# Kernel optimization log

Hardware: AMD Instinct MI355X
Metric: run time of the kernel (lower is better)

## Reference

```python
import jax, jax.numpy as jnp
import numpy as np

DIM = 384
HEADS = 6
K = 3  # kernel_size, stride = 1


def setup_inputs() -> dict:
    key = jax.random.key(0)
    ks = jax.random.split(key, 7)
    B, H, W, C = 16, 56, 56, DIM
    sc = 1.0 / np.sqrt(C)
    return {
        "x_map": jax.random.normal(ks[0], (B, H, W, C), dtype=jnp.float32),
        # Linear weights stored [in, out] (torch stores [out, in]; math identical)
        "W_attn": jax.random.normal(ks[1], (C, HEADS * K * K), dtype=jnp.float32) * sc,
        "b_attn": jax.random.normal(ks[2], (HEADS * K * K,), dtype=jnp.float32) * 0.02,
        "W_v": jax.random.normal(ks[3], (C, C), dtype=jnp.float32) * sc,
        "b_v": jax.random.normal(ks[4], (C,), dtype=jnp.float32) * 0.02,
        "W_proj": jax.random.normal(ks[5], (C, C), dtype=jnp.float32) * sc,
        "b_proj": jax.random.normal(ks[6], (C,), dtype=jnp.float32) * 0.02,
    }


def reference(x_map, W_attn, b_attn, W_v, b_v, W_proj, b_proj):
    B, H, W, C = x_map.shape
    k, heads = K, HEADS
    hd = C // heads
    pad = k // 2

    # attention logits per output pixel: [B, H*W, heads, k*k], softmax over window
    a = x_map @ W_attn + b_attn                     # [B,H,W,heads*k*k]
    a = jax.nn.softmax(a.reshape(B, H * W, heads, k * k), axis=-1)

    v = x_map @ W_v + b_v                           # [B,H,W,C]
    vp = jnp.pad(v, ((0, 0), (pad, pad), (pad, pad), (0, 0)))
    # k*k shifted views == F.unfold with row-major (ki,kj) kernel order
    patches = jnp.stack(
        [vp[:, i:i + H, j:j + W, :] for i in range(k) for j in range(k)],
        axis=3,
    )                                               # [B,H,W,k*k,C]
    patches = patches.reshape(B, H * W, k * k, heads, hd)

    # softmax-weighted sum over the k*k window, per head
    y = jnp.einsum('bpKhd,bphK->bphd', patches, a)  # [B,H*W,heads,hd]
    y = y.reshape(B, H, W, C)
    return y @ W_proj + b_proj
```

## Files before the change

kernel.cpp:

```cpp
#include <hip/hip_runtime.h>
#include <math.h>

#define NPIX 50176
#define CDIM 384
#define HEADS 6
#define NLOGIT 54
#define HH 56
#define WW 56

typedef __attribute__((ext_vector_type(8))) __bf16 bf16x8;
typedef __attribute__((ext_vector_type(4))) float f32x4;

__device__ __forceinline__ void glds16(const void* g, void* l) {
  __builtin_amdgcn_global_load_lds(
      (const __attribute__((address_space(1))) unsigned int*)g,
      (__attribute__((address_space(3))) unsigned int*)l, 16, 0, 0);
}

__global__ __launch_bounds__(256) void prep_kernel(
    const float* __restrict__ W_v, const float* __restrict__ W_proj,
    const float* __restrict__ W_attn, const float* __restrict__ b_attn,
    __bf16* __restrict__ Wtv, __bf16* __restrict__ Wtp,
    __bf16* __restrict__ Wta, float* __restrict__ bpad) {
  const int idx = blockIdx.x * 256 + threadIdx.x;
  const int WSZ = CDIM * CDIM;
  if (idx < WSZ) {
    const int n = idx / CDIM, k = idx % CDIM;
    Wtv[idx] = (__bf16)W_v[k * CDIM + n];
    Wtp[idx] = (__bf16)W_proj[k * CDIM + n];
  } else if (idx < WSZ + 64 * CDIM) {
    const int r = idx - WSZ;
    const int n = r / CDIM, k = r % CDIM;
    Wta[r] = (__bf16)((n < NLOGIT) ? W_attn[k * NLOGIT + n] : 0.f);
  } else if (idx < WSZ + 64 * CDIM + 64) {
    const int n = idx - WSZ - 64 * CDIM;
    bpad[n] = (n < NLOGIT) ? b_attn[n] : 0.f;
  }
}

__global__ __launch_bounds__(256) void cast_x_kernel(
    const float* __restrict__ x, __bf16* __restrict__ xb) {
  const size_t i = (size_t)blockIdx.x * 256 + threadIdx.x;
  const float4* src = (const float4*)x + i * 4;
  const float4 f0 = src[0];
  const float4 f1 = src[1];
  const float4 f2 = src[2];
  const float4 f3 = src[3];
  bf16x8 o0, o1;
  o0[0] = (__bf16)f0.x; o0[1] = (__bf16)f0.y; o0[2] = (__bf16)f0.z; o0[3] = (__bf16)f0.w;
  o0[4] = (__bf16)f1.x; o0[5] = (__bf16)f1.y; o0[6] = (__bf16)f1.z; o0[7] = (__bf16)f1.w;
  o1[0] = (__bf16)f2.x; o1[1] = (__bf16)f2.y; o1[2] = (__bf16)f2.z; o1[3] = (__bf16)f2.w;
  o1[4] = (__bf16)f3.x; o1[5] = (__bf16)f3.y; o1[6] = (__bf16)f3.z; o1[7] = (__bf16)f3.w;
  ((bf16x8*)xb)[i * 2]     = o0;
  ((bf16x8*)xb)[i * 2 + 1] = o1;
}

__global__ __launch_bounds__(256) void gemm_v_logit_kernel(
    const __bf16* __restrict__ xb, const __bf16* __restrict__ Wtv,
    const float* __restrict__ b_v, __bf16* __restrict__ v,
    const __bf16* __restrict__ Wta, const float* __restrict__ bpad,
    float* __restrict__ attn) {
  __shared__ char smem[34816];
  __bf16 (*As)[32] = (__bf16(*)[32])smem;
  __bf16 (*Bs)[32] = (__bf16(*)[32])(smem + 8192);
  float (*Ls)[68]  = (float(*)[68])smem;

  const int tid  = threadIdx.x;
  const int wave = tid >> 6;
  const int lane = tid & 63;
  const int bm   = blockIdx.x * 128;
  const int lrow  = lane >> 2;
  const int lkoff = (lane & 3) * 8;
  const int frow  = lane & 15;
  const int fk    = (lane >> 4) * 8;

  if (blockIdx.y < 3) {
    const int bn = blockIdx.y * 128;
    const int wr = (wave >> 1) * 64;
    const int wc = (wave & 1) * 64;
    f32x4 acc[4][4] = {};

    for (int k0 = 0; k0 < CDIM; k0 += 32) {
      const __bf16* ga = xb  + (size_t)(bm + wave * 32 + lrow) * CDIM + k0 + lkoff;
      const __bf16* gb = Wtv + (size_t)(bn + wave * 32 + lrow) * CDIM + k0 + lkoff;
      glds16(ga,                     &As[wave * 32][0]);
      glds16(ga + 16 * (size_t)CDIM, &As[wave * 32 + 16][0]);
      glds16(gb,                     &Bs[wave * 32][0]);
      glds16(gb + 16 * (size_t)CDIM, &Bs[wave * 32 + 16][0]);
      __syncthreads();

      bf16x8 a[4], b[4];
      #pragma unroll
      for (int mi = 0; mi < 4; ++mi)
        a[mi] = *(const bf16x8*)&As[wr + mi * 16 + frow][fk];
      #pragma unroll
      for (int ni = 0; ni < 4; ++ni)
        b[ni] = *(const bf16x8*)&Bs[wc + ni * 16 + frow][fk];
      #pragma unroll
      for (int mi = 0; mi < 4; ++mi)
        #pragma unroll
        for (int ni = 0; ni < 4; ++ni)
          acc[mi][ni] = __builtin_amdgcn_mfma_f32_16x16x32_bf16(
              a[mi], b[ni], acc[mi][ni], 0, 0, 0);
      __syncthreads();
    }

    const int orow = (lane >> 4) * 4;
    #pragma unroll
    for (int mi = 0; mi < 4; ++mi) {
      #pragma unroll
      for (int ni = 0; ni < 4; ++ni) {
        const int n = bn + wc + ni * 16 + frow;
        const float bvl = b_v[n];
        #pragma unroll
        for (int r = 0; r < 4; ++r) {
          const int m = bm + wr + mi * 16 + orow + r;
          v[(size_t)m * CDIM + n] = (__bf16)(acc[mi][ni][r] + bvl);
        }
      }
    }
  } else {
    f32x4 acc[2][4] = {};

    for (int k0 = 0; k0 < CDIM; k0 += 32) {
      const __bf16* ga = xb  + (size_t)(bm + wave * 32 + lrow) * CDIM + k0 + lkoff;
      const __bf16* gb = Wta + (size_t)(wave * 16 + lrow) * CDIM + k0 + lkoff;
      glds16(ga,                     &As[wave * 32][0]);
      glds16(ga + 16 * (size_t)CDIM, &As[wave * 32 + 16][0]);
      glds16(gb,                     &Bs[wave * 16][0]);
      __syncthreads();

      bf16x8 a[2], b[4];
      #pragma unroll
      for (int mi = 0; mi < 2; ++mi)
        a[mi] = *(const bf16x8*)&As[wave * 32 + mi * 16 + frow][fk];
      #pragma unroll
      for (int ni = 0; ni < 4; ++ni)
        b[ni] = *(const bf16x8*)&Bs[ni * 16 + frow][fk];
      #pragma unroll
      for (int mi = 0; mi < 2; ++mi)
        #pragma unroll
        for (int ni = 0; ni < 4; ++ni)
          acc[mi][ni] = __builtin_amdgcn_mfma_f32_16x16x32_bf16(
              a[mi], b[ni], acc[mi][ni], 0, 0, 0);
      __syncthreads();
    }

    float bvl[4];
    #pragma unroll
    for (int ni = 0; ni < 4; ++ni) bvl[ni] = bpad[ni * 16 + frow];
    const int orow = (lane >> 4) * 4;
    #pragma unroll
    for (int mi = 0; mi < 2; ++mi)
      #pragma unroll
      for (int ni = 0; ni < 4; ++ni)
        #pragma unroll
        for (int r = 0; r < 4; ++r)
          Ls[wave * 32 + mi * 16 + orow + r][ni * 16 + frow] =
              acc[mi][ni][r] + bvl[ni];
    __syncthreads();

    #pragma unroll
    for (int it = 0; it < 3; ++it) {
      const int task = it * 256 + tid;
      const int pl = task / HEADS;
      const int h  = task % HEADS;
      const float* row = &Ls[pl][h * 9];
      float m = row[0];
      #pragma unroll
      for (int w = 1; w < 9; ++w) m = fmaxf(m, row[w]);
      float e[9], s = 0.f;
      #pragma unroll
      for (int w = 0; w < 9; ++w) { e[w] = __expf(row[w] - m); s += e[w]; }
      const float inv = 1.f / s;
      float* op = &attn[(size_t)(bm + pl) * NLOGIT + h * 9];
      #pragma unroll
      for (int w = 0; w < 9; ++w) op[w] = e[w] * inv;
    }
  }
}

__global__ __launch_bounds__(256) void gemm_proj_kernel(
    const __bf16* __restrict__ A, const __bf16* __restrict__ Bt,
    const float* __restrict__ bias, float* __restrict__ Out) {
  __shared__ __bf16 As[128][32];
  __shared__ __bf16 Bs[128][32];

  const int tid  = threadIdx.x;
  const int wave = tid >> 6;
  const int lane = tid & 63;
  const int bm = blockIdx.x * 128;
  const int bn = blockIdx.y * 128;

  const int lrow  = lane >> 2;
  const int lkoff = (lane & 3) * 8;
  const int frow  = lane & 15;
  const int fk    = (lane >> 4) * 8;
  const int wr = (wave >> 1) * 64;
  const int wc = (wave & 1) * 64;

  f32x4 acc[4][4] = {};

  for (int k0 = 0; k0 < CDIM; k0 += 32) {
    const __bf16* ga = A  + (size_t)(bm + wave * 32 + lrow) * CDIM + k0 + lkoff;
    const __bf16* gb = Bt + (size_t)(bn + wave * 32 + lrow) * CDIM + k0 + lkoff;
    glds16(ga,                     &As[wave * 32][0]);
    glds16(ga + 16 * (size_t)CDIM, &As[wave * 32 + 16][0]);
    glds16(gb,                     &Bs[wave * 32][0]);
    glds16(gb + 16 * (size_t)CDIM, &Bs[wave * 32 + 16][0]);
    __syncthreads();

    bf16x8 a[4], b[4];
    #pragma unroll
    for (int mi = 0; mi < 4; ++mi)
      a[mi] = *(const bf16x8*)&As[wr + mi * 16 + frow][fk];
    #pragma unroll
    for (int ni = 0; ni < 4; ++ni)
      b[ni] = *(const bf16x8*)&Bs[wc + ni * 16 + frow][fk];
    #pragma unroll
    for (int mi = 0; mi < 4; ++mi)
      #pragma unroll
      for (int ni = 0; ni < 4; ++ni)
        acc[mi][ni] = __builtin_amdgcn_mfma_f32_16x16x32_bf16(
            a[mi], b[ni], acc[mi][ni], 0, 0, 0);
    __syncthreads();
  }

  const int orow = (lane >> 4) * 4;
  #pragma unroll
  for (int mi = 0; mi < 4; ++mi) {
    #pragma unroll
    for (int ni = 0; ni < 4; ++ni) {
      const int n = bn + wc + ni * 16 + frow;
      const float bvl = bias[n];
      #pragma unroll
      for (int r = 0; r < 4; ++r) {
        const int m = bm + wr + mi * 16 + orow + r;
        Out[(size_t)m * CDIM + n] = acc[mi][ni][r] + bvl;
      }
    }
  }
}

__global__ __launch_bounds__(256) void aggregate_kernel(
    const __bf16* __restrict__ v, const float* __restrict__ attn,
    __bf16* __restrict__ y) {
  const int idx = blockIdx.x * 256 + threadIdx.x;
  const int cg = idx % 48;
  const int pg = idx / 48;
  const int c  = cg * 8;
  const int b  = pg / ((HH / 4) * WW);
  const int r2 = pg % ((HH / 4) * WW);
  const int i0 = (r2 / WW) * 4;
  const int j  = r2 % WW;
  const int head = c >> 6;

  const int pbase = (b * HH + i0) * WW + j;
  float aw[4][9];
  #pragma unroll
  for (int p = 0; p < 4; ++p) {
    const float* ap = attn + (size_t)(pbase + p * WW) * NLOGIT + head * 9;
    #pragma unroll
    for (int w = 0; w < 9; ++w) aw[p][w] = ap[w];
  }

  const bool j0ok = (j > 0), j2ok = (j < WW - 1);
  float acc[4][8] = {};

  #pragma unroll
  for (int li = 0; li < 6; ++li) {
    const int ii = i0 - 1 + li;
    if (ii < 0 || ii >= HH) continue;
    const __bf16* vrow = v + ((size_t)(b * HH + ii) * WW + j) * CDIM + c;
    float ch[3][8];
    #pragma unroll
    for (int kj = 0; kj < 3; ++kj) {
      const bool ok = (kj == 0) ? j0ok : (kj == 2) ? j2ok : true;
      if (ok) {
        const bf16x8 vv = *(const bf16x8*)(vrow + (kj - 1) * CDIM);
        #pragma unroll
        for (int q = 0; q < 8; ++q) ch[kj][q] = (float)vv[q];
      } else {
        #pragma unroll
        for (int q = 0; q < 8; ++q) ch[kj][q] = 0.f;
      }
    }
    #pragma unroll
    for (int p = 0; p < 4; ++p) {
      const int ki = li - p;
      if (ki < 0 || ki > 2) continue;
      #pragma unroll
      for (int kj = 0; kj < 3; ++kj) {
        const float w = aw[p][ki * 3 + kj];
        #pragma unroll
        for (int q = 0; q < 8; ++q) acc[p][q] += w * ch[kj][q];
      }
    }
  }

  #pragma unroll
  for (int p = 0; p < 4; ++p) {
    bf16x8 o;
    #pragma unroll
    for (int q = 0; q < 8; ++q) o[q] = (__bf16)acc[p][q];
    *(bf16x8*)&y[(size_t)(pbase + p * WW) * CDIM + c] = o;
  }
}

extern "C" void kernel_launch(void* const* d_in, const int* in_sizes, int n_in,
                              void* d_out, int out_size, void* d_ws,
                              size_t ws_size, hipStream_t stream) {
  const float* x      = (const float*)d_in[0];
  const float* W_attn = (const float*)d_in[1];
  const float* b_attn = (const float*)d_in[2];
  const float* W_v    = (const float*)d_in[3];
  const float* b_v    = (const float*)d_in[4];
  const float* W_proj = (const float*)d_in[5];
  const float* b_proj = (const float*)d_in[6];
  float* out = (float*)d_out;

  char* w = (char*)d_ws;
  __bf16* xb   = (__bf16*)w;  w += (size_t)NPIX * CDIM * 2;
  __bf16* v    = (__bf16*)w;  w += (size_t)NPIX * CDIM * 2;
  __bf16* y    = (__bf16*)w;  w += (size_t)NPIX * CDIM * 2;
  float*  attn = (float*)w;   w += (size_t)NPIX * NLOGIT * 4;
  __bf16* Wta  = (__bf16*)w;  w += 64 * CDIM * 2;
  float*  bpad = (float*)w;   w += 64 * 4;
  __bf16* Wtv  = (__bf16*)w;  w += CDIM * CDIM * 2;
  __bf16* Wtp  = (__bf16*)w;  w += CDIM * CDIM * 2;

  const int prep_n = CDIM * CDIM + 64 * CDIM + 64;
  prep_kernel<<<(prep_n + 255) / 256, 256, 0, stream>>>(
      W_v, W_proj, W_attn, b_attn, Wtv, Wtp, Wta, bpad);

  cast_x_kernel<<<(NPIX * CDIM / 16) / 256, 256, 0, stream>>>(x, xb);

  gemm_v_logit_kernel<<<dim3(NPIX / 128, 4), 256, 0, stream>>>(
      xb, Wtv, b_v, v, Wta, bpad, attn);

  aggregate_kernel<<<(NPIX / 4 * 48) / 256, 256, 0, stream>>>(v, attn, y);

  gemm_proj_kernel<<<dim3(NPIX / 128, CDIM / 128), 256, 0, stream>>>(
      y, Wtp, b_proj, out);
}
```

Measured before the change: 119.7 us.

## Fuse window aggregation into projection GEMM A-tile construction

Removes the separate aggregate kernel and the intermediate y buffer by computing each softmax-weighted 3x3 window sum directly into the shared-memory A tile of the projection GEMM. This saves a full write and read of the bf16 y tensor and one kernel launch. In exchange, the aggregation is recomputed once per output-column block (three times) and the neighbor gathers sit on the GEMM critical path without row reuse.

```diff
diff --git a/kernel.cpp b/kernel.cpp
--- a/kernel.cpp
+++ b/kernel.cpp
@@ -180,9 +180,10 @@
   }
 }
 
-__global__ __launch_bounds__(256) void gemm_proj_kernel(
-    const __bf16* __restrict__ A, const __bf16* __restrict__ Bt,
-    const float* __restrict__ bias, float* __restrict__ Out) {
+__global__ __launch_bounds__(256) void gemm_proj_agg_kernel(
+    const __bf16* __restrict__ v, const float* __restrict__ attn,
+    const __bf16* __restrict__ Bt, const float* __restrict__ bias,
+    float* __restrict__ Out) {
   __shared__ __bf16 As[128][32];
   __shared__ __bf16 Bs[128][32];
 
@@ -199,15 +200,64 @@
   const int wr = (wave >> 1) * 64;
   const int wc = (wave & 1) * 64;
 
+  const int px0 = tid >> 2;
+  const int cg  = tid & 3;
+  int ibase[2], jpos[2];
+  size_t vbase[2];
+  #pragma unroll
+  for (int t = 0; t < 2; ++t) {
+    const int p = bm + px0 + t * 64;
+    const int bimg = p / (HH * WW);
+    const int rem  = p % (HH * WW);
+    ibase[t] = rem / WW;
+    jpos[t]  = rem % WW;
+    vbase[t] = ((size_t)(bimg * HH + ibase[t]) * WW + jpos[t]) * CDIM;
+  }
+
+  float aw[2][9];
   f32x4 acc[4][4] = {};
 
-  for (int k0 = 0; k0 < CDIM; k0 += 32) {
-    const __bf16* ga = A  + (size_t)(bm + wave * 32 + lrow) * CDIM + k0 + lkoff;
+  for (int ks = 0; ks < 12; ++ks) {
+    const int k0 = ks * 32;
     const __bf16* gb = Bt + (size_t)(bn + wave * 32 + lrow) * CDIM + k0 + lkoff;
-    glds16(ga,                     &As[wave * 32][0]);
-    glds16(ga + 16 * (size_t)CDIM, &As[wave * 32 + 16][0]);
     glds16(gb,                     &Bs[wave * 32][0]);
     glds16(gb + 16 * (size_t)CDIM, &Bs[wave * 32 + 16][0]);
+
+    if ((ks & 1) == 0) {
+      const int head = k0 >> 6;
+      #pragma unroll
+      for (int t = 0; t < 2; ++t) {
+        const int p = bm + px0 + t * 64;
+        const float* ap = attn + (size_t)p * NLOGIT + head * 9;
+        #pragma unroll
+        for (int w = 0; w < 9; ++w) aw[t][w] = ap[w];
+      }
+    }
+
+    #pragma unroll
+    for (int t = 0; t < 2; ++t) {
+      const int i = ibase[t], j = jpos[t];
+      float a8[8] = {};
+      #pragma unroll
+      for (int ki = 0; ki < 3; ++ki) {
+        const int ii = i + ki - 1;
+        if (ii < 0 || ii >= HH) continue;
+        #pragma unroll
+        for (int kj = 0; kj < 3; ++kj) {
+          const int jj = j + kj - 1;
+          if (jj < 0 || jj >= WW) continue;
+          const float wgt = aw[t][ki * 3 + kj];
+          const bf16x8 vv = *(const bf16x8*)&v[
+              vbase[t] + ((ii - i) * WW + (jj - j)) * CDIM + k0 + cg * 8];
+          #pragma unroll
+          for (int q = 0; q < 8; ++q) a8[q] += wgt * (float)vv[q];
+        }
+      }
+      bf16x8 o;
+      #pragma unroll
+      for (int q = 0; q < 8; ++q) o[q] = (__bf16)a8[q];
+      *(bf16x8*)&As[px0 + t * 64][cg * 8] = o;
+    }
     __syncthreads();
 
     bf16x8 a[4], b[4];
@@ -239,71 +289,6 @@
         Out[(size_t)m * CDIM + n] = acc[mi][ni][r] + bvl;
       }
     }
-  }
-}
-
-__global__ __launch_bounds__(256) void aggregate_kernel(
-    const __bf16* __restrict__ v, const float* __restrict__ attn,
-    __bf16* __restrict__ y) {
-  const int idx = blockIdx.x * 256 + threadIdx.x;
-  const int cg = idx % 48;
-  const int pg = idx / 48;
-  const int c  = cg * 8;
-  const int b  = pg / ((HH / 4) * WW);
-  const int r2 = pg % ((HH / 4) * WW);
-  const int i0 = (r2 / WW) * 4;
-  const int j  = r2 % WW;
-  const int head = c >> 6;
-
-  const int pbase = (b * HH + i0) * WW + j;
-  float aw[4][9];
-  #pragma unroll
-  for (int p = 0; p < 4; ++p) {
-    const float* ap = attn + (size_t)(pbase + p * WW) * NLOGIT + head * 9;
-    #pragma unroll
-    for (int w = 0; w < 9; ++w) aw[p][w] = ap[w];
-  }
-
-  const bool j0ok = (j > 0), j2ok = (j < WW - 1);
-  float acc[4][8] = {};
-
-  #pragma unroll
-  for (int li = 0; li < 6; ++li) {
-    const int ii = i0 - 1 + li;
-    if (ii < 0 || ii >= HH) continue;
-    const __bf16* vrow = v + ((size_t)(b * HH + ii) * WW + j) * CDIM + c;
-    float ch[3][8];
-    #pragma unroll
-    for (int kj = 0; kj < 3; ++kj) {
-      const bool ok = (kj == 0) ? j0ok : (kj == 2) ? j2ok : true;
-      if (ok) {
-        const bf16x8 vv = *(const bf16x8*)(vrow + (kj - 1) * CDIM);
-        #pragma unroll
-        for (int q = 0; q < 8; ++q) ch[kj][q] = (float)vv[q];
-      } else {
-        #pragma unroll
-        for (int q = 0; q < 8; ++q) ch[kj][q] = 0.f;
-      }
-    }
-    #pragma unroll
-    for (int p = 0; p < 4; ++p) {
-      const int ki = li - p;
-      if (ki < 0 || ki > 2) continue;
-      #pragma unroll
-      for (int kj = 0; kj < 3; ++kj) {
-        const float w = aw[p][ki * 3 + kj];
-        #pragma unroll
-        for (int q = 0; q < 8; ++q) acc[p][q] += w * ch[kj][q];
-      }
-    }
-  }
-
-  #pragma unroll
-  for (int p = 0; p < 4; ++p) {
-    bf16x8 o;
-    #pragma unroll
-    for (int q = 0; q < 8; ++q) o[q] = (__bf16)acc[p][q];
-    *(bf16x8*)&y[(size_t)(pbase + p * WW) * CDIM + c] = o;
   }
 }
 
@@ -322,7 +307,6 @@
   char* w = (char*)d_ws;
   __bf16* xb   = (__bf16*)w;  w += (size_t)NPIX * CDIM * 2;
   __bf16* v    = (__bf16*)w;  w += (size_t)NPIX * CDIM * 2;
-  __bf16* y    = (__bf16*)w;  w += (size_t)NPIX * CDIM * 2;
   float*  attn = (float*)w;   w += (size_t)NPIX * NLOGIT * 4;
   __bf16* Wta  = (__bf16*)w;  w += 64 * CDIM * 2;
   float*  bpad = (float*)w;   w += 64 * 4;
@@ -338,8 +322,6 @@
   gemm_v_logit_kernel<<<dim3(NPIX / 128, 4), 256, 0, stream>>>(
       xb, Wtv, b_v, v, Wta, bpad, attn);
 
-  aggregate_kernel<<<(NPIX / 4 * 48) / 256, 256, 0, stream>>>(v, attn, y);
-
-  gemm_proj_kernel<<<dim3(NPIX / 128, CDIM / 128), 256, 0, stream>>>(
-      y, Wtp, b_proj, out);
-}
+  gemm_proj_agg_kernel<<<dim3(NPIX / 128, CDIM / 128), 256, 0, stream>>>(
+      v, attn, Wtp, b_proj, out);
+}
```

Measured after the change: 253.2 us. 112% more time.
